# Kernel tuning notes

Hardware: AMD Instinct MI355X
Metric: run time of the kernel (lower is better)

## Reference

```python
import jax, jax.numpy as jnp
import numpy as np

B = 4096; NINP = 512; NHID = 2048; NB = 8; BS = 256  # block_size_out
ATT_OUT = 4 * BS; TOPK = 4; DK_I = 64; NH = 4; DK_M = 16


def setup_inputs() -> dict:
    ks = jax.random.split(jax.random.key(0), 16)
    g = lambda i, shape, s=0.01: s * jax.random.normal(ks[i], shape, dtype=jnp.float32)
    return dict(
        inp=jax.random.normal(ks[0], (B, NINP), dtype=jnp.float32),
        hx=jax.random.normal(ks[1], (B, NHID), dtype=jnp.float32),
        cx=jax.random.normal(ks[2], (B, NHID), dtype=jnp.float32),
        # inp_att group-linear projections (GroupLinearLayer init 0.01*randn)
        Wq_i=g(3, (NB, BS, DK_I)), Wk_i=g(4, (2, NINP, DK_I)), Wv_i=g(5, (2, NINP, ATT_OUT)),
        # mha group-linear projections (4 heads * d_k=16)
        Wq_m=g(6, (NB, BS, NH * DK_M)), Wk_m=g(7, (NB, BS, NH * DK_M)), Wv_m=g(8, (NB, BS, NH * DK_M)),
        fc_w=g(9, (BS, NH * DK_M), 0.05), fc_b=jnp.zeros((BS,), jnp.float32),
        gate_w=g(10, (BS, NH * DK_M), 0.05), gate_b=jnp.zeros((BS,), jnp.float32),
        # blockified LSTMCell: k=NB independent (ATT_OUT -> BS) cells, gate order i,f,g,o
        Wih=g(11, (NB, 4 * BS, ATT_OUT), 0.02), Whh=g(12, (NB, 4 * BS, BS), 0.05),
        b_ih=jnp.zeros((NB, 4 * BS), jnp.float32), b_hh=jnp.zeros((NB, 4 * BS), jnp.float32),
        step=0,
    )


def _fwd(inp, hx, cx, Wq_i, Wk_i, Wv_i, Wq_m, Wk_m, Wv_m, fc_w, fc_b, gate_w, gate_b, Wih, Whh, b_ih, b_hh):
    b = inp.shape[0]
    # input read: concat null slot + input (num_blocks_in=1, num_modules_read_input=2)
    x = inp.reshape(b, 1, NINP)
    x = jnp.concatenate([jnp.zeros_like(x), x], axis=1)  # (b, 2, NINP); slot 0 = null
    hq = hx.reshape(b, NB, BS)
    q = jnp.einsum('bkd,kde->bke', hq, Wq_i)              # (b, NB, DK_I)
    k = jnp.einsum('bkd,kde->bke', x, Wk_i)               # (b, 2, DK_I)
    v = jnp.einsum('bkd,kde->bke', x, Wv_i)               # (b, 2, ATT_OUT)
    iatt = jax.nn.softmax(jnp.einsum('bqe,bke->bqk', q, k) / jnp.sqrt(jnp.float32(DK_I)), axis=-1)
    inp_use = jnp.einsum('bqk,bke->bqe', iatt, v)         # (b, NB, ATT_OUT); skip_write => identity fc
    # top-k selection: blocks with HIGHEST null-attention get frozen (masked out)
    _, botk = jax.lax.top_k(iatt[:, :, 0], NB - TOPK)
    mblk = jnp.ones((b, NB), inp.dtype).at[jnp.arange(b)[:, None], botk].set(0.0)
    mblk = jax.lax.stop_gradient(mblk)                    # mask.detach()
    mask = jnp.repeat(mblk, BS, axis=1)                   # (b, NHID)
    # block-diagonal LSTM cell (post blockify_params)
    hb = hx.reshape(b, NB, BS); cb = cx.reshape(b, NB, BS)
    gates = jnp.einsum('bkd,kgd->bkg', inp_use, Wih) + jnp.einsum('bkh,kgh->bkg', hb, Whh) + b_ih + b_hh
    ig, fg, gg, og = jnp.split(gates, 4, axis=-1)
    c_new = jax.nn.sigmoid(fg) * cb + jax.nn.sigmoid(ig) * jnp.tanh(gg)
    h_new = jax.nn.sigmoid(og) * jnp.tanh(c_new)          # (b, NB, BS)
    # step attention among blocks; blocked_grad: forward identity, backward masked
    m3 = mblk[:, :, None]
    hg = m3 * h_new + jax.lax.stop_gradient((1.0 - m3) * h_new)
    qm = jnp.einsum('bkd,kde->bke', hg, Wq_m).reshape(b, NB, NH, DK_M)
    km = jnp.einsum('bkd,kde->bke', hg, Wk_m).reshape(b, NB, NH, DK_M)
    vm = jnp.einsum('bkd,kde->bke', hg, Wv_m).reshape(b, NB, NH, DK_M)
    a = jax.nn.softmax(jnp.einsum('bqhe,bkhe->bhqk', qm, km) / jnp.sqrt(jnp.float32(DK_M)), axis=-1)
    o = jnp.einsum('bhqk,bkhe->bqhe', a, vm).reshape(b, NB, NH * DK_M)
    att_out = jax.nn.sigmoid(o @ gate_w.T + gate_b) * jnp.tanh(o @ fc_w.T + fc_b)  # residual gating
    h_new = (h_new + att_out).reshape(b, NHID)
    c_new = c_new.reshape(b, NHID)
    hx_out = mask * h_new + (1.0 - mask) * hx
    cx_out = mask * c_new + (1.0 - mask) * cx
    return hx_out, cx_out, mask


def reference(inp, hx, cx, Wq_i, Wk_i, Wv_i, Wq_m, Wk_m, Wv_m, fc_w, fc_b, gate_w, gate_b, Wih, Whh, b_ih, b_hh, step):
    return _fwd(inp, hx, cx, Wq_i, Wk_i, Wv_i, Wq_m, Wk_m, Wv_m, fc_w, fc_b, gate_w, gate_b, Wih, Whh, b_ih, b_hh)
```

## Files before the change

kernel.cpp:

```cpp
#include <hip/hip_runtime.h>
#include <hip/hip_bf16.h>


#define B_SZ 4096
#define NINP 512
#define NHID 2048
#define NB 8
#define BSZ 256
#define ATT_OUT 1024

typedef __attribute__((ext_vector_type(8))) short bf16x8;
typedef __attribute__((ext_vector_type(8))) unsigned short u16x8;
typedef __attribute__((ext_vector_type(4))) float f32x4;

__device__ __forceinline__ float sigf(float x) { return 1.0f / (1.0f + expf(-x)); }

__device__ __forceinline__ unsigned short f2bf(float x) {
    unsigned u = __float_as_uint(x);
    unsigned r = (u + 0x7fff + ((u >> 16) & 1)) >> 16;
    return (unsigned short)r;
}
__device__ __forceinline__ float bf2f(unsigned short u) {
    return __uint_as_float((unsigned)u << 16);
}

__device__ __forceinline__ void gload16(const void* g, void* l) {
    __builtin_amdgcn_global_load_lds(
        (const __attribute__((address_space(1))) unsigned int*)(unsigned long long)g,
        (__attribute__((address_space(3))) unsigned int*)(unsigned int)(unsigned long long)l,
        16, 0, 0);
}

__device__ __forceinline__ u16x8 cvt8(const float4& a, const float4& b) {
    u16x8 v;
    v[0] = f2bf(a.x); v[1] = f2bf(a.y); v[2] = f2bf(a.z); v[3] = f2bf(a.w);
    v[4] = f2bf(b.x); v[5] = f2bf(b.y); v[6] = f2bf(b.z); v[7] = f2bf(b.w);
    return v;
}

__global__ __launch_bounds__(256) void prep1_kernel(
    const float* __restrict__ gw, const float* __restrict__ fw,
    unsigned short* __restrict__ Wgfb,
    const float4* __restrict__ hx4, u16x8* __restrict__ hxb8,
    const float4* __restrict__ inp4, u16x8* __restrict__ inpb8,
    const float* __restrict__ WvSrc, unsigned short* __restrict__ Wvb)
{
    __shared__ float tile[32][33];
    const int bid = blockIdx.x;
    if (bid < 128) {
        int t = bid * 256 + threadIdx.x;
        Wgfb[t] = f2bf((t < 16384) ? gw[t] : fw[t - 16384]);
    } else if (bid < 4224) {
        long i = (long)(bid - 128) * 256 + threadIdx.x;
        hxb8[i] = cvt8(hx4[i * 2], hx4[i * 2 + 1]);
    } else if (bid < 5248) {
        long i = (long)(bid - 4224) * 256 + threadIdx.x;
        inpb8[i] = cvt8(inp4[i * 2], inp4[i * 2 + 1]);
    } else {
        const int b2 = bid - 5248;
        const int n0 = (b2 & 31) * 32;
        const int k0 = (b2 >> 5) * 32;
        const int tx = threadIdx.x & 31;
        const int ty = threadIdx.x >> 5;
        #pragma unroll
        for (int r = 0; r < 4; ++r)
            tile[ty + r * 8][tx] = WvSrc[(long)(k0 + ty + r * 8) * 1024 + n0 + tx];
        __syncthreads();
        #pragma unroll
        for (int r = 0; r < 4; ++r)
            Wvb[(long)(n0 + ty + r * 8) * 512 + k0 + tx] = f2bf(tile[tx][ty + r * 8]);
    }
}

__global__ __launch_bounds__(256) void prepW_kernel(
    const float4* __restrict__ Wih4, u16x8* __restrict__ Wihb8,
    const float4* __restrict__ Whh4, u16x8* __restrict__ Whhb8)
{
    const int bid = blockIdx.x;
    if (bid < 4096) {
        long i = (long)bid * 256 + threadIdx.x;
        Wihb8[i] = cvt8(Wih4[i * 2], Wih4[i * 2 + 1]);
    } else {
        long i = (long)(bid - 4096) * 256 + threadIdx.x;
        Whhb8[i] = cvt8(Whh4[i * 2], Whh4[i * 2 + 1]);
    }
}

__global__ __launch_bounds__(256) void qkvw_kernel(
    const float* __restrict__ Wq, const float* __restrict__ Wk,
    const float* __restrict__ Wv, unsigned short* __restrict__ out)
{
    int idx = blockIdx.x * 256 + threadIdx.x;
    int k = idx & 255;
    int n = (idx >> 8) % 192;
    int kb = idx / (192 * 256);
    const float* src = (n < 64) ? Wq : (n < 128) ? Wk : Wv;
    int nn = n & 63;
    out[idx] = f2bf(src[(long)kb * 16384 + k * 64 + nn]);
}

__global__ __launch_bounds__(256) void qk1_kernel(
    const float* __restrict__ inp, const float* __restrict__ hx,
    const float* __restrict__ Wk1, const float* __restrict__ Wq,
    float* __restrict__ k1, float* __restrict__ q)
{
    const int role = blockIdx.y;
    const int m0 = blockIdx.x * 32;
    const float* A; long lda; const float* Bw; int K; float* C; int ldc;
    if (role == 8) {
        A = inp + (long)m0 * 512; lda = 512; Bw = Wk1; K = 512;
        C = k1 + (long)m0 * 64; ldc = 64;
    } else {
        A = hx + (long)m0 * 2048 + role * 256; lda = 2048;
        Bw = Wq + (long)role * 256 * 64; K = 256;
        C = q + (long)m0 * 512 + role * 64; ldc = 512;
    }

    __shared__ float As[32][33];
    __shared__ float Bs[32][64];

    const int t = threadIdx.x;
    const int ty = t >> 4;
    const int tx = t & 15;

    float acc[2][4] = {};

    for (int k0 = 0; k0 < K; k0 += 32) {
        {
            int m = t >> 3, kk = (t & 7) << 2;
            float4 av = *reinterpret_cast<const float4*>(&A[(long)m * lda + k0 + kk]);
            As[m][kk] = av.x; As[m][kk + 1] = av.y;
            As[m][kk + 2] = av.z; As[m][kk + 3] = av.w;
        }
        #pragma unroll
        for (int u = 0; u < 2; ++u) {
            int f = t + 256 * u;
            int kr = f >> 4, c = (f & 15) << 2;
            float4 bv = *reinterpret_cast<const float4*>(&Bw[(long)(k0 + kr) * 64 + c]);
            *reinterpret_cast<float4*>(&Bs[kr][c]) = bv;
        }
        __syncthreads();
        #pragma unroll
        for (int kk = 0; kk < 32; ++kk) {
            float a0 = As[ty * 2][kk];
            float a1 = As[ty * 2 + 1][kk];
            float4 bv = *reinterpret_cast<const float4*>(&Bs[kk][tx * 4]);
            acc[0][0] += a0 * bv.x; acc[0][1] += a0 * bv.y;
            acc[0][2] += a0 * bv.z; acc[0][3] += a0 * bv.w;
            acc[1][0] += a1 * bv.x; acc[1][1] += a1 * bv.y;
            acc[1][2] += a1 * bv.z; acc[1][3] += a1 * bv.w;
        }
        __syncthreads();
    }
    #pragma unroll
    for (int i = 0; i < 2; ++i) {
        float4 v = {acc[i][0], acc[i][1], acc[i][2], acc[i][3]};
        *reinterpret_cast<float4*>(&C[(long)(ty * 2 + i) * ldc + tx * 4]) = v;
    }
}

__global__ __launch_bounds__(256, 2) void gemm_mfma_bf(
    const unsigned short* __restrict__ A,
    const unsigned short* __restrict__ Bm,
    unsigned short* __restrict__ Cv,
    int K, int lda, int ldb, int ldc,
    long aOffZ, long bOffZ, long cOffZ)
{
    const int m0 = blockIdx.x * 128;
    const int n0 = blockIdx.y * 64;
    const int z = blockIdx.z;
    A += (long)z * aOffZ;
    Bm += (long)z * bOffZ;

    __shared__ unsigned short As[128 * 64];
    __shared__ unsigned short Bs[64 * 64];

    const int t = threadIdx.x;
    const int wid = t >> 6;
    const int l = t & 63;
    const int l15 = l & 15;
    const int l4 = l >> 4;
    const int wm = wid >> 1;
    const int wn = wid & 1;

    f32x4 acc[4][2];
    #pragma unroll
    for (int m = 0; m < 4; ++m)
        #pragma unroll
        for (int n = 0; n < 2; ++n)
            acc[m][n] = (f32x4){0.f, 0.f, 0.f, 0.f};

    for (int k0 = 0; k0 < K; k0 += 64) {
        #pragma unroll
        for (int s = 0; s < 4; ++s) {
            int ci = (wid * 4 + s) * 64 + l;
            int r = ci >> 3, cs = ci & 7;
            gload16(A + (long)(m0 + r) * lda + k0 + ((cs ^ (r & 7)) << 3), &As[ci * 8]);
        }
        #pragma unroll
        for (int s = 0; s < 2; ++s) {
            int ci = (wid * 2 + s) * 64 + l;
            int rn = ci >> 3, cs = ci & 7;
            gload16(Bm + (long)(n0 + rn) * ldb + k0 + ((cs ^ (rn & 7)) << 3), &Bs[ci * 8]);
        }
        __syncthreads();
        #pragma unroll
        for (int kh = 0; kh < 2; ++kh) {
            bf16x8 af[4];
            #pragma unroll
            for (int m = 0; m < 4; ++m) {
                int r = wm * 64 + m * 16 + l15;
                int c = kh * 4 + l4;
                af[m] = *reinterpret_cast<const bf16x8*>(&As[r * 64 + ((c ^ (r & 7)) << 3)]);
            }
            #pragma unroll
            for (int nf = 0; nf < 2; ++nf) {
                int rn = wn * 32 + nf * 16 + l15;
                int c = kh * 4 + l4;
                bf16x8 bf = *reinterpret_cast<const bf16x8*>(
                    &Bs[rn * 64 + ((c ^ (rn & 7)) << 3)]);
                #pragma unroll
                for (int m = 0; m < 4; ++m)
                    acc[m][nf] = __builtin_amdgcn_mfma_f32_16x16x32_bf16(
                        af[m], bf, acc[m][nf], 0, 0, 0);
            }
        }
        __syncthreads();
    }

    #pragma unroll
    for (int nf = 0; nf < 2; ++nf) {
        const int ccol = n0 + wn * 32 + nf * 16 + l15;
        #pragma unroll
        for (int m = 0; m < 4; ++m) {
            #pragma unroll
            for (int r = 0; r < 4; ++r) {
                const long crow = m0 + wm * 64 + m * 16 + l4 * 4 + r;
                Cv[(long)z * cOffZ + crow * ldc + ccol] = f2bf(acc[m][nf][r]);
            }
        }
    }
}

__global__ __launch_bounds__(256) void s1_mask_kernel(
    const float* __restrict__ q, const float* __restrict__ k1,
    float* __restrict__ w_ws, float* __restrict__ mblk,
    float* __restrict__ mask_out)
{
    const int wave = threadIdx.x >> 6;
    const int lane = threadIdx.x & 63;
    const int b = blockIdx.x * 4 + wave;

    float p[8];
    const float kv = k1[(long)b * 64 + lane];
    #pragma unroll
    for (int kb = 0; kb < 8; ++kb)
        p[kb] = q[(long)b * 512 + kb * 64 + lane] * kv;

    #pragma unroll
    for (int off = 1; off < 64; off <<= 1) {
        #pragma unroll
        for (int kb = 0; kb < 8; ++kb) p[kb] += __shfl_xor(p[kb], off);
    }

    float s[8], mv[8];
    #pragma unroll
    for (int kb = 0; kb < 8; ++kb) s[kb] = p[kb] * 0.125f;

    #pragma unroll
    for (int j = 0; j < 8; ++j) {
        int r = 0;
        #pragma unroll
        for (int i = 0; i < 8; ++i)
            r += (s[i] < s[j]) || (s[i] == s[j] && i < j);
        mv[j] = (r >= 4) ? 1.0f : 0.0f;
    }
    if (lane < 8) {
        w_ws[(long)b * 8 + lane] = sigf(s[lane]);
        mblk[(long)b * 8 + lane] = mv[lane];
    }
    #pragma unroll
    for (int it = 0; it < 8; ++it) {
        const float mvv = mv[it];
        float4 v = {mvv, mvv, mvv, mvv};
        *reinterpret_cast<float4*>(&mask_out[(long)b * 2048 + it * 256 + lane * 4]) = v;
    }
}

__global__ __launch_bounds__(256, 2) void gates_mfma_kernel(
    const unsigned short* __restrict__ Ab,
    const unsigned short* __restrict__ Hb,
    const unsigned short* __restrict__ Wihb,
    const unsigned short* __restrict__ Whhb,
    const float* __restrict__ b_ih, const float* __restrict__ b_hh,
    const float* __restrict__ w_ws, const float* __restrict__ mblk,
    const float* __restrict__ cx,
    float* __restrict__ c_out,
    unsigned short* __restrict__ hn_b)
{
    const int n = blockIdx.x + 32 * blockIdx.y + 128 * blockIdx.z;
    const int w = (n & 7) * 128 + (n >> 3);
    const int m0 = ((w >> 2) & 31) * 128;
    const int j0 = (w & 3) * 64;
    const int kb = w >> 7;

    __shared__ unsigned short As[128 * 64];
    __shared__ unsigned short Bs[256 * 64];
    __shared__ float wv[128];
    __shared__ float mbs[128];

    const int t = threadIdx.x;
    const int wid = t >> 6;
    const int l = t & 63;
    const int l15 = l & 15;
    const int l4 = l >> 4;
    const int wm = wid >> 1;
    const int wj = wid & 1;

    if (t < 128) {
        wv[t] = w_ws[(long)(m0 + t) * 8 + kb];
        mbs[t] = mblk[(long)(m0 + t) * 8 + kb];
    }

    f32x4 acc[4][8];
    #pragma unroll
    for (int m = 0; m < 4; ++m)
        #pragma unroll
        for (int nn = 0; nn < 8; ++nn)
            acc[m][nn] = (f32x4){0.f, 0.f, 0.f, 0.f};

    auto stage = [&](const unsigned short* Aptr, long lda,
                     const unsigned short* Bptr, long ldb, int k0) {
        #pragma unroll
        for (int s = 0; s < 4; ++s) {
            int ci = (wid * 4 + s) * 64 + l;
            int r = ci >> 3, cs = ci & 7;
            const unsigned short* g = Aptr + (long)r * lda + k0 + ((cs ^ (r & 7)) << 3);
            gload16(g, &As[ci * 8]);
        }
        #pragma unroll
        for (int s = 0; s < 8; ++s) {
            int ci = (wid * 8 + s) * 64 + l;
            int rn = ci >> 3, cs = ci & 7;
            int sg = rn >> 6, jl = rn & 63;
            const unsigned short* g = Bptr + (long)(sg * 256 + j0 + jl) * ldb + k0
                                      + ((cs ^ (rn & 7)) << 3);
            gload16(g, &Bs[ci * 8]);
        }
    };

    auto compute = [&]() {
        #pragma unroll
        for (int kh = 0; kh < 2; ++kh) {
            bf16x8 af[4];
            #pragma unroll
            for (int m = 0; m < 4; ++m) {
                int r = wm * 64 + m * 16 + l15;
                int c = kh * 4 + l4;
                af[m] = *reinterpret_cast<const bf16x8*>(&As[r * 64 + ((c ^ (r & 7)) << 3)]);
            }
            #pragma unroll
            for (int sg = 0; sg < 4; ++sg) {
                #pragma unroll
                for (int jf = 0; jf < 2; ++jf) {
                    int rn = sg * 64 + wj * 32 + jf * 16 + l15;
                    int c = kh * 4 + l4;
                    bf16x8 bf = *reinterpret_cast<const bf16x8*>(
                        &Bs[rn * 64 + ((c ^ (rn & 7)) << 3)]);
                    #pragma unroll
                    for (int m = 0; m < 4; ++m)
                        acc[m][sg * 2 + jf] = __builtin_amdgcn_mfma_f32_16x16x32_bf16(
                            af[m], bf, acc[m][sg * 2 + jf], 0, 0, 0);
                }
            }
        }
    };

    {
        const unsigned short* A1 = Ab + (long)m0 * 1024;
        const unsigned short* B1 = Wihb + (long)kb * 1024 * 1024;
        for (int k0 = 0; k0 < 1024; k0 += 64) {
            stage(A1, 1024, B1, 1024, k0);
            __syncthreads();
            compute();
            __syncthreads();
        }
    }

    {
        float wsc[4][4];
        #pragma unroll
        for (int m = 0; m < 4; ++m)
            #pragma unroll
            for (int r = 0; r < 4; ++r)
                wsc[m][r] = wv[wm * 64 + m * 16 + l4 * 4 + r];
        #pragma unroll
        for (int m = 0; m < 4; ++m)
            #pragma unroll
            for (int nn = 0; nn < 8; ++nn)
                #pragma unroll
                for (int r = 0; r < 4; ++r)
                    acc[m][nn][r] *= wsc[m][r];
    }

    {
        const unsigned short* A2 = Hb + (long)m0 * 2048 + kb * 256;
        const unsigned short* B2 = Whhb + (long)kb * 1024 * 256;
        for (int k0 = 0; k0 < 256; k0 += 64) {
            stage(A2, 2048, B2, 256, k0);
            __syncthreads();
            compute();
            __syncthreads();
        }
    }

    #pragma unroll
    for (int jf = 0; jf < 2; ++jf) {
        const int jcol = j0 + wj * 32 + jf * 16 + l15;
        const long bb = (long)kb * 1024 + jcol;
        const float bI = b_ih[bb] + b_hh[bb];
        const float bF = b_ih[bb + 256] + b_hh[bb + 256];
        const float bG = b_ih[bb + 512] + b_hh[bb + 512];
        const float bO = b_ih[bb + 768] + b_hh[bb + 768];
        #pragma unroll
        for (int m = 0; m < 4; ++m) {
            #pragma unroll
            for (int r = 0; r < 4; ++r) {
                const long row = m0 + wm * 64 + m * 16 + l4 * 4 + r;
                const long idx = row * 2048 + kb * 256 + jcol;
                const float mv = mbs[wm * 64 + m * 16 + l4 * 4 + r];
                const float ig = acc[m][0 + jf][r] + bI;
                const float fg = acc[m][2 + jf][r] + bF;
                const float gg = acc[m][4 + jf][r] + bG;
                const float og = acc[m][6 + jf][r] + bO;
                const float co = cx[idx];
                const float cn = sigf(fg) * co + sigf(ig) * tanhf(gg);
                const float hn = sigf(og) * tanhf(cn);
                c_out[idx] = (mv != 0.0f) ? cn : co;
                hn_b[idx] = f2bf(hn);
            }
        }
    }
}

__global__ __launch_bounds__(256) void attn_m2_kernel(
    const unsigned short* __restrict__ qkv, unsigned short* __restrict__ ob)
{
    const int tid = blockIdx.x * 256 + threadIdx.x;
    const int b = tid >> 5;
    const int qkb = (tid >> 2) & 7;
    const int h = tid & 3;
    const unsigned short* base = qkv + (long)b * 1536;

    float qv[16];
    {
        const unsigned short* qp = base + qkb * 192 + h * 16;
        #pragma unroll
        for (int e = 0; e < 16; ++e) qv[e] = bf2f(qp[e]);
    }

    float sc[8];
    float mx = -1e30f;
    #pragma unroll
    for (int kk = 0; kk < 8; ++kk) {
        const unsigned short* kp = base + kk * 192 + 64 + h * 16;
        float s = 0.f;
        #pragma unroll
        for (int e = 0; e < 16; ++e) s += qv[e] * bf2f(kp[e]);
        s *= 0.25f;
        sc[kk] = s;
        mx = fmaxf(mx, s);
    }
    float den = 0.f;
    #pragma unroll
    for (int kk = 0; kk < 8; ++kk) { sc[kk] = expf(sc[kk] - mx); den += sc[kk]; }
    const float inv = 1.0f / den;

    float ov[16] = {};
    #pragma unroll
    for (int kk = 0; kk < 8; ++kk) {
        const float pw = sc[kk] * inv;
        const unsigned short* vp = base + kk * 192 + 128 + h * 16;
        #pragma unroll
        for (int e = 0; e < 16; ++e) ov[e] += pw * bf2f(vp[e]);
    }
    u16x8 r0, r1;
    #pragma unroll
    for (int e = 0; e < 8; ++e) { r0[e] = f2bf(ov[e]); r1[e] = f2bf(ov[e + 8]); }
    unsigned short* op = ob + (long)((b * 8 + qkb) * 64 + h * 16);
    *reinterpret_cast<u16x8*>(op) = r0;
    *reinterpret_cast<u16x8*>(op + 8) = r1;
}

__global__ __launch_bounds__(256) void attn_final_kernel(
    const unsigned short* __restrict__ ob,
    const unsigned short* __restrict__ Wgfb,
    const float* __restrict__ gate_b, const float* __restrict__ fc_b,
    const float* __restrict__ mblk,
    const float* __restrict__ hx,
    const unsigned short* __restrict__ hnb,
    float* __restrict__ h_out)
{
    const int m0 = blockIdx.x * 128;
    const int j0 = blockIdx.y * 64;

    __shared__ unsigned short As[128 * 64];
    __shared__ unsigned short Bs[128 * 64];

    const int t = threadIdx.x;
    const int wid = t >> 6;
    const int l = t & 63;
    const int l15 = l & 15;
    const int l4 = l >> 4;
    const int wm = wid >> 1;
    const int wn = wid & 1;

    #pragma unroll
    for (int s = 0; s < 4; ++s) {
        int ci = (wid * 4 + s) * 64 + l;
        int r = ci >> 3, cs = ci & 7;
        gload16(ob + (long)(m0 + r) * 64 + ((cs ^ (r & 7)) << 3), &As[ci * 8]);
    }
    #pragma unroll
    for (int s = 0; s < 4; ++s) {
        int ci = (wid * 4 + s) * 64 + l;
        int r = ci >> 3, cs = ci & 7;
        int n = (r < 64) ? (j0 + r) : (256 + j0 + (r - 64));
        gload16(Wgfb + (long)n * 64 + ((cs ^ (r & 7)) << 3), &Bs[ci * 8]);
    }
    __syncthreads();

    f32x4 acc[4][2][2];
    #pragma unroll
    for (int m = 0; m < 4; ++m)
        #pragma unroll
        for (int nf = 0; nf < 2; ++nf)
            #pragma unroll
            for (int gf = 0; gf < 2; ++gf)
                acc[m][nf][gf] = (f32x4){0.f, 0.f, 0.f, 0.f};

    #pragma unroll
    for (int kh = 0; kh < 2; ++kh) {
        const int c = kh * 4 + l4;
        bf16x8 af[4];
        #pragma unroll
        for (int m = 0; m < 4; ++m) {
            int r = wm * 64 + m * 16 + l15;
            af[m] = *reinterpret_cast<const bf16x8*>(&As[r * 64 + ((c ^ (r & 7)) << 3)]);
        }
        #pragma unroll
        for (int nf = 0; nf < 2; ++nf) {
            int rg = wn * 32 + nf * 16 + l15;
            bf16x8 bg = *reinterpret_cast<const bf16x8*>(
                &Bs[rg * 64 + ((c ^ (rg & 7)) << 3)]);
            int rf = 64 + rg;
            bf16x8 bfv = *reinterpret_cast<const bf16x8*>(
                &Bs[rf * 64 + ((c ^ (rf & 7)) << 3)]);
            #pragma unroll
            for (int m = 0; m < 4; ++m) {
                acc[m][nf][0] = __builtin_amdgcn_mfma_f32_16x16x32_bf16(
                    af[m], bg, acc[m][nf][0], 0, 0, 0);
                acc[m][nf][1] = __builtin_amdgcn_mfma_f32_16x16x32_bf16(
                    af[m], bfv, acc[m][nf][1], 0, 0, 0);
            }
        }
    }

    #pragma unroll
    for (int nf = 0; nf < 2; ++nf) {
        const int j = j0 + wn * 32 + nf * 16 + l15;
        const float gb = gate_b[j];
        const float fb = fc_b[j];
        #pragma unroll
        for (int m = 0; m < 4; ++m) {
            #pragma unroll
            for (int r = 0; r < 4; ++r) {
                const long p = m0 + wm * 64 + m * 16 + l4 * 4 + r;
                const float g = acc[m][nf][0][r] + gb;
                const float f = acc[m][nf][1][r] + fb;
                const float att = sigf(g) * tanhf(f);
                const long idx = (p >> 3) * 2048 + (p & 7) * 256 + j;
                const float mv = mblk[p];
                const float hn = bf2f(hnb[idx]) + att;
                h_out[idx] = (mv != 0.0f) ? hn : hx[idx];
            }
        }
    }
}

extern "C" void kernel_launch(void* const* d_in, const int* in_sizes, int n_in,
                              void* d_out, int out_size, void* d_ws, size_t ws_size,
                              hipStream_t stream) {
    const float* inp    = (const float*)d_in[0];
    const float* hx     = (const float*)d_in[1];
    const float* cx     = (const float*)d_in[2];
    const float* Wq_i   = (const float*)d_in[3];
    const float* Wk_i   = (const float*)d_in[4];
    const float* Wv_i   = (const float*)d_in[5];
    const float* Wq_m   = (const float*)d_in[6];
    const float* Wk_m   = (const float*)d_in[7];
    const float* Wv_m   = (const float*)d_in[8];
    const float* fc_w   = (const float*)d_in[9];
    const float* fc_b   = (const float*)d_in[10];
    const float* gate_w = (const float*)d_in[11];
    const float* gate_b = (const float*)d_in[12];
    const float* Wih    = (const float*)d_in[13];
    const float* Whh    = (const float*)d_in[14];
    const float* b_ih   = (const float*)d_in[15];
    const float* b_hh   = (const float*)d_in[16];

    float* out      = (float*)d_out;
    float* h_out    = out;
    float* c_out    = out + (long)B_SZ * 2048;
    float* mask_out = out + (long)2 * B_SZ * 2048;

    float* ws   = (float*)d_ws;
    float* w_ws = ws;
    float* mblk = w_ws + (long)B_SZ * 8;
    unsigned short* v1b = (unsigned short*)(mblk + (long)B_SZ * 8);
    unsigned short* hxb = v1b + (long)B_SZ * 1024;
    unsigned short* hnb  = hxb + (long)B_SZ * 2048;
    unsigned short* Wihb = hnb + (long)B_SZ * 2048;
    unsigned short* Whhb = Wihb + (long)8 * 1024 * 1024;
    unsigned short* Wgfb = Whhb + (long)8 * 1024 * 256;
    float* k1 = (float*)Wihb;
    float* q  = k1 + (long)B_SZ * 64;
    unsigned short* inpb = (unsigned short*)(q + (long)B_SZ * 512);
    unsigned short* Wvb  = inpb + (long)B_SZ * 512;
    unsigned short* Wqkvb = Wihb;
    unsigned short* qkvb  = hxb;
    unsigned short* ob    = v1b;

    prep1_kernel<<<dim3(5760), 256, 0, stream>>>(
        gate_w, fc_w, Wgfb,
        (const float4*)hx, (u16x8*)hxb,
        (const float4*)inp, (u16x8*)inpb,
        Wv_i + (long)NINP * ATT_OUT, Wvb);
    qk1_kernel<<<dim3(128, 9), 256, 0, stream>>>(
        inp, hx, Wk_i + (long)NINP * 64, Wq_i, k1, q);
    gemm_mfma_bf<<<dim3(32, 16, 1), 256, 0, stream>>>(
        inpb, Wvb, v1b, 512, 512, 512, 1024, 0, 0, 0);
    s1_mask_kernel<<<dim3(B_SZ / 4), 256, 0, stream>>>(q, k1, w_ws, mblk, mask_out);
    prepW_kernel<<<dim3(5120), 256, 0, stream>>>(
        (const float4*)Wih, (u16x8*)Wihb, (const float4*)Whh, (u16x8*)Whhb);
    gates_mfma_kernel<<<dim3(B_SZ / 128, 4, 8), 256, 0, stream>>>(
        v1b, hxb, Wihb, Whhb, b_ih, b_hh, w_ws, mblk, cx, c_out, hnb);
    qkvw_kernel<<<dim3(1536), 256, 0, stream>>>(Wq_m, Wk_m, Wv_m, Wqkvb);
    gemm_mfma_bf<<<dim3(32, 3, 8), 256, 0, stream>>>(
        hnb, Wqkvb, qkvb, 256, 2048, 256, 1536, 256, (long)192 * 256, 192);
    attn_m2_kernel<<<dim3(B_SZ * 32 / 256), 256, 0, stream>>>(qkvb, ob);
    attn_final_kernel<<<dim3(256, 4), 256, 0, stream>>>(
        ob, Wgfb, gate_b, fc_b, mblk, hx, hnb, h_out);
}
```

Measured before the change: 262.0 us.

## Fold Wv projection into Wih weights to shrink gates GEMM K dimension

Instead of computing v1 = inp·Wv (B×1024) and then multiplying it by Wih (K=1024), the code precomputes a fused weight Gt = Wih·Wv per block (1024×512) with a batched GEMM. The gates kernel then multiplies the bf16 input directly by Gt with K=512, halving the input-side reduction and removing the v1 intermediate. The Wv transpose in prep1 becomes a plain conversion, and workspace is remapped, with inpb placed in h_out. The attention kernel also switches to 16-byte vector loads of q/k/v. The change risks extra bf16 rounding from the fused weights and adds a weight-only GEMM to every call.

```diff
diff --git a/kernel.cpp b/kernel.cpp
--- a/kernel.cpp
+++ b/kernel.cpp
@@ -43,9 +43,8 @@
     unsigned short* __restrict__ Wgfb,
     const float4* __restrict__ hx4, u16x8* __restrict__ hxb8,
     const float4* __restrict__ inp4, u16x8* __restrict__ inpb8,
-    const float* __restrict__ WvSrc, unsigned short* __restrict__ Wvb)
-{
-    __shared__ float tile[32][33];
+    const float4* __restrict__ Wv4, u16x8* __restrict__ Wvb8)
+{
     const int bid = blockIdx.x;
     if (bid < 128) {
         int t = bid * 256 + threadIdx.x;
@@ -57,18 +56,8 @@
         long i = (long)(bid - 4224) * 256 + threadIdx.x;
         inpb8[i] = cvt8(inp4[i * 2], inp4[i * 2 + 1]);
     } else {
-        const int b2 = bid - 5248;
-        const int n0 = (b2 & 31) * 32;
-        const int k0 = (b2 >> 5) * 32;
-        const int tx = threadIdx.x & 31;
-        const int ty = threadIdx.x >> 5;
-        #pragma unroll
-        for (int r = 0; r < 4; ++r)
-            tile[ty + r * 8][tx] = WvSrc[(long)(k0 + ty + r * 8) * 1024 + n0 + tx];
-        __syncthreads();
-        #pragma unroll
-        for (int r = 0; r < 4; ++r)
-            Wvb[(long)(n0 + ty + r * 8) * 512 + k0 + tx] = f2bf(tile[tx][ty + r * 8]);
+        long i = (long)(bid - 5248) * 256 + threadIdx.x;
+        Wvb8[i] = cvt8(Wv4[i * 2], Wv4[i * 2 + 1]);
     }
 }
 
@@ -288,9 +277,9 @@
 }
 
 __global__ __launch_bounds__(256, 2) void gates_mfma_kernel(
-    const unsigned short* __restrict__ Ab,
+    const unsigned short* __restrict__ Ib,
     const unsigned short* __restrict__ Hb,
-    const unsigned short* __restrict__ Wihb,
+    const unsigned short* __restrict__ Gt,
     const unsigned short* __restrict__ Whhb,
     const float* __restrict__ b_ih, const float* __restrict__ b_hh,
     const float* __restrict__ w_ws, const float* __restrict__ mblk,
@@ -377,10 +366,10 @@
     };
 
     {
-        const unsigned short* A1 = Ab + (long)m0 * 1024;
-        const unsigned short* B1 = Wihb + (long)kb * 1024 * 1024;
-        for (int k0 = 0; k0 < 1024; k0 += 64) {
-            stage(A1, 1024, B1, 1024, k0);
+        const unsigned short* A1 = Ib + (long)m0 * 512;
+        const unsigned short* B1 = Gt + (long)kb * 1024 * 512;
+        for (int k0 = 0; k0 < 512; k0 += 64) {
+            stage(A1, 512, B1, 512, k0);
             __syncthreads();
             compute();
             __syncthreads();
@@ -450,23 +439,26 @@
     const int b = tid >> 5;
     const int qkb = (tid >> 2) & 7;
     const int h = tid & 3;
-    const unsigned short* base = qkv + (long)b * 1536;
+    const u16x8* base8 = reinterpret_cast<const u16x8*>(qkv + (long)b * 1536);
 
     float qv[16];
     {
-        const unsigned short* qp = base + qkb * 192 + h * 16;
-        #pragma unroll
-        for (int e = 0; e < 16; ++e) qv[e] = bf2f(qp[e]);
+        u16x8 q0 = base8[qkb * 24 + h * 2];
+        u16x8 q1 = base8[qkb * 24 + h * 2 + 1];
+        #pragma unroll
+        for (int e = 0; e < 8; ++e) { qv[e] = bf2f(q0[e]); qv[8 + e] = bf2f(q1[e]); }
     }
 
     float sc[8];
     float mx = -1e30f;
     #pragma unroll
     for (int kk = 0; kk < 8; ++kk) {
-        const unsigned short* kp = base + kk * 192 + 64 + h * 16;
+        u16x8 k0 = base8[kk * 24 + 8 + h * 2];
+        u16x8 k1 = base8[kk * 24 + 9 + h * 2];
         float s = 0.f;
         #pragma unroll
-        for (int e = 0; e < 16; ++e) s += qv[e] * bf2f(kp[e]);
+        for (int e = 0; e < 8; ++e)
+            s += qv[e] * bf2f(k0[e]) + qv[8 + e] * bf2f(k1[e]);
         s *= 0.25f;
         sc[kk] = s;
         mx = fmaxf(mx, s);
@@ -480,9 +472,13 @@
     #pragma unroll
     for (int kk = 0; kk < 8; ++kk) {
         const float pw = sc[kk] * inv;
-        const unsigned short* vp = base + kk * 192 + 128 + h * 16;
-        #pragma unroll
-        for (int e = 0; e < 16; ++e) ov[e] += pw * bf2f(vp[e]);
+        u16x8 v0 = base8[kk * 24 + 16 + h * 2];
+        u16x8 v1 = base8[kk * 24 + 17 + h * 2];
+        #pragma unroll
+        for (int e = 0; e < 8; ++e) {
+            ov[e] += pw * bf2f(v0[e]);
+            ov[8 + e] += pw * bf2f(v1[e]);
+        }
     }
     u16x8 r0, r1;
     #pragma unroll
@@ -617,34 +613,35 @@
     float* ws   = (float*)d_ws;
     float* w_ws = ws;
     float* mblk = w_ws + (long)B_SZ * 8;
-    unsigned short* v1b = (unsigned short*)(mblk + (long)B_SZ * 8);
-    unsigned short* hxb = v1b + (long)B_SZ * 1024;
+    unsigned short* Gt  = (unsigned short*)(mblk + (long)B_SZ * 8);
+    unsigned short* hxb = Gt + (long)8 * 1024 * 512;
     unsigned short* hnb  = hxb + (long)B_SZ * 2048;
     unsigned short* Wihb = hnb + (long)B_SZ * 2048;
     unsigned short* Whhb = Wihb + (long)8 * 1024 * 1024;
     unsigned short* Wgfb = Whhb + (long)8 * 1024 * 256;
     float* k1 = (float*)Wihb;
     float* q  = k1 + (long)B_SZ * 64;
-    unsigned short* inpb = (unsigned short*)(q + (long)B_SZ * 512);
-    unsigned short* Wvb  = inpb + (long)B_SZ * 512;
+    unsigned short* Wvb = hnb;
+    unsigned short* inpb = (unsigned short*)h_out;
     unsigned short* Wqkvb = Wihb;
     unsigned short* qkvb  = hxb;
-    unsigned short* ob    = v1b;
-
-    prep1_kernel<<<dim3(5760), 256, 0, stream>>>(
+    unsigned short* ob    = (unsigned short*)Gt;
+
+    prep1_kernel<<<dim3(5504), 256, 0, stream>>>(
         gate_w, fc_w, Wgfb,
         (const float4*)hx, (u16x8*)hxb,
         (const float4*)inp, (u16x8*)inpb,
-        Wv_i + (long)NINP * ATT_OUT, Wvb);
+        (const float4*)(Wv_i + (long)NINP * ATT_OUT), (u16x8*)Wvb);
     qk1_kernel<<<dim3(128, 9), 256, 0, stream>>>(
         inp, hx, Wk_i + (long)NINP * 64, Wq_i, k1, q);
-    gemm_mfma_bf<<<dim3(32, 16, 1), 256, 0, stream>>>(
-        inpb, Wvb, v1b, 512, 512, 512, 1024, 0, 0, 0);
     s1_mask_kernel<<<dim3(B_SZ / 4), 256, 0, stream>>>(q, k1, w_ws, mblk, mask_out);
     prepW_kernel<<<dim3(5120), 256, 0, stream>>>(
         (const float4*)Wih, (u16x8*)Wihb, (const float4*)Whh, (u16x8*)Whhb);
+    gemm_mfma_bf<<<dim3(8, 8, 8), 256, 0, stream>>>(
+        Wihb, Wvb, Gt, 1024, 1024, 1024, 512,
+        (long)1024 * 1024, 0, (long)1024 * 512);
     gates_mfma_kernel<<<dim3(B_SZ / 128, 4, 8), 256, 0, stream>>>(
-        v1b, hxb, Wihb, Whhb, b_ih, b_hh, w_ws, mblk, cx, c_out, hnb);
+        inpb, hxb, Gt, Whhb, b_ih, b_hh, w_ws, mblk, cx, c_out, hnb);
     qkvw_kernel<<<dim3(1536), 256, 0, stream>>>(Wq_m, Wk_m, Wv_m, Wqkvb);
     gemm_mfma_bf<<<dim3(32, 3, 8), 256, 0, stream>>>(
         hnb, Wqkvb, qkvb, 256, 2048, 256, 1536, 256, (long)192 * 256, 192);
```

After: 235.0 us. 1.11x faster.
